# Optimization experiments

Hardware: AMD Instinct MI355X
Metric: run time of the kernel (lower is better)

The kernel has to match this reference:

```python
import jax, jax.numpy as jnp
import numpy as np

B, J, D = 512, 22, 3
HIDDEN = 512
OUT = J * D          # 66, flattened frame size
NCLS = 12
LENGTH = 64


def setup_inputs() -> dict:
    key = jax.random.key(0)
    ks = jax.random.split(key, 12)
    s = 0.05
    return {
        "inputs": jax.random.normal(ks[0], (B, J, D), dtype=jnp.float32),
        "labels": jax.random.randint(ks[1], (B,), 0, NCLS),
        "length": LENGTH,
        # LSTMCell params (torch layout: W_ih [4H, in], W_hh [4H, H], gate order i,f,g,o)
        "W_ih": jax.random.normal(ks[2], (4 * HIDDEN, OUT + NCLS), dtype=jnp.float32) * s,
        "W_hh": jax.random.normal(ks[3], (4 * HIDDEN, HIDDEN), dtype=jnp.float32) * s,
        "b_ih": jax.random.normal(ks[4], (4 * HIDDEN,), dtype=jnp.float32) * s,
        "b_hh": jax.random.normal(ks[5], (4 * HIDDEN,), dtype=jnp.float32) * s,
        # fc: hidden -> output
        "W_fc": jax.random.normal(ks[6], (OUT, HIDDEN), dtype=jnp.float32) * s,
        "b_fc": jax.random.normal(ks[7], (OUT,), dtype=jnp.float32) * s,
        # fc_inh / fc_inc: output -> hidden (initial state projections)
        "W_inh": jax.random.normal(ks[8], (HIDDEN, OUT), dtype=jnp.float32) * s,
        "b_inh": jax.random.normal(ks[9], (HIDDEN,), dtype=jnp.float32) * s,
        "W_inc": jax.random.normal(ks[10], (HIDDEN, OUT), dtype=jnp.float32) * s,
        "b_inc": jax.random.normal(ks[11], (HIDDEN,), dtype=jnp.float32) * s,
    }


def reference(inputs, labels, length, W_ih, W_hh, b_ih, b_hh, W_fc, b_fc,
              W_inh, b_inh, W_inc, b_inc):
    b, j, d = inputs.shape
    enc = jax.nn.one_hot(labels, NCLS, dtype=inputs.dtype)      # [B, NCLS]
    frame0 = inputs.reshape(b, j * d)                            # [B, OUT]
    h0 = frame0 @ W_inh.T + b_inh                                # [B, H]
    c0 = frame0 @ W_inc.T + b_inc                                # [B, H]
    frame = jnp.concatenate([frame0, enc], axis=-1)              # [B, OUT+NCLS]

    def step(carry, _):
        h, c, fr = carry
        gates = fr @ W_ih.T + b_ih + h @ W_hh.T + b_hh           # [B, 4H]
        i, f, g, o = jnp.split(gates, 4, axis=-1)                # torch gate order
        c_new = jax.nn.sigmoid(f) * c + jax.nn.sigmoid(i) * jnp.tanh(g)
        h_new = jax.nn.sigmoid(o) * jnp.tanh(c_new)
        out = h_new @ W_fc.T + b_fc                              # [B, OUT]
        fr_new = jnp.concatenate([out, enc], axis=-1)
        return (h_new, c_new, fr_new), out

    _, outs = jax.lax.scan(step, (h0, c0, frame), None, length=length)  # [L, B, OUT]
    return jnp.transpose(outs, (1, 0, 2)).reshape(b, length, j, d)
```

## Files before the change

### kernel.cpp

```cpp
#include <hip/hip_runtime.h>

#define OUTD 66
#define INW  78
#define FH   2048
#define LEN  64

typedef short bf16x8 __attribute__((ext_vector_type(8)));
typedef float f32x4  __attribute__((ext_vector_type(4)));
typedef unsigned int u32x4 __attribute__((ext_vector_type(4)));

__device__ __forceinline__ float bf2f(unsigned short u) {
  union { unsigned int i; float f; } v; v.i = ((unsigned int)u) << 16; return v.f;
}
__device__ __forceinline__ unsigned short f2bf(float f) {
  union { float f; unsigned int i; } v; v.f = f;
  unsigned int u = v.i;
  return (unsigned short)((u + 0x7fffu + ((u >> 16) & 1u)) >> 16);
}
__device__ __forceinline__ float sigm(float x) { return 1.f / (1.f + __expf(-x)); }
__device__ __forceinline__ float tanh_f(float x) { return 2.f / (1.f + __expf(-2.f * x)) - 1.f; }

__global__ __launch_bounds__(256) void k_initA(
    const float* __restrict__ W_hh, const float* __restrict__ W_ih,
    const float* __restrict__ W_fc, const float* __restrict__ b_ih,
    const float* __restrict__ b_hh, const float* __restrict__ b_fc,
    const float* __restrict__ inp, const float* __restrict__ W_inh,
    const float* __restrict__ b_inh, const float* __restrict__ W_inc,
    const float* __restrict__ b_inc,
    unsigned short* __restrict__ Weff, float* __restrict__ bias_eff,
    unsigned short* __restrict__ hbuf, float* __restrict__ c0,
    unsigned short* __restrict__ Wfc16, unsigned int* __restrict__ flags,
    unsigned int* __restrict__ flagsL)
{
  int tid = threadIdx.x, bid = blockIdx.x;
  if (bid < 256) {
    int nb = bid;
    int k = tid * 2;
    float acc[8][2];
    #pragma unroll
    for (int r = 0; r < 8; ++r) {
      int n = nb * 8 + r;
      acc[r][0] = W_hh[n * 512 + k];
      acc[r][1] = W_hh[n * 512 + k + 1];
    }
    for (int m = 0; m < OUTD; ++m) {
      float w0 = W_fc[m * 512 + k];
      float w1 = W_fc[m * 512 + k + 1];
      #pragma unroll
      for (int r = 0; r < 8; ++r) {
        float wih = W_ih[(nb * 8 + r) * INW + m];
        acc[r][0] += wih * w0;
        acc[r][1] += wih * w1;
      }
    }
    #pragma unroll
    for (int r = 0; r < 8; ++r) {
      int n = nb * 8 + r;
      unsigned int pack = (unsigned int)f2bf(acc[r][0]) | ((unsigned int)f2bf(acc[r][1]) << 16);
      *(unsigned int*)(Weff + n * 512 + k) = pack;
    }
    if (tid < 8) {
      int n = nb * 8 + tid;
      float a = b_ih[n] + b_hh[n];
      for (int m = 0; m < OUTD; ++m) a += b_fc[m] * W_ih[n * INW + m];
      bias_eff[n] = a;
    }
    if (nb == 0) {
      for (int i = tid; i < 512 * 16; i += 256) flags[i] = 0;
      for (int i = tid; i < 256 * 16; i += 256) flagsL[i] = 0;
    }
  } else {
    int nb = bid - 256;
    for (int r = 0; r < 2; ++r) {
      int b = nb * 2 + r;
      for (int half = 0; half < 2; ++half) {
        int c = tid + half * 256;
        float ha = b_inh[c], ca = b_inc[c];
        for (int m = 0; m < OUTD; ++m) {
          float f = inp[b * OUTD + m];
          ha += f * W_inh[c * OUTD + m];
          ca += f * W_inc[c * OUTD + m];
        }
        hbuf[((b >> 6) * 32 + (c >> 4)) * 1024 + (b & 63) * 16 + (c & 15)] = f2bf(ha);
        c0[b * 512 + c] = ca;
      }
    }
    if (nb == 0) {
      for (int i = tid; i < OUTD * 512; i += 256) Wfc16[i] = f2bf(W_fc[i]);
    }
  }
}

__global__ __launch_bounds__(128) void k_init2a(
    const float* __restrict__ inp, const unsigned short* __restrict__ hbuf,
    const float* __restrict__ W_fc, const float* __restrict__ b_fc,
    float* __restrict__ d0)
{
  int b = blockIdx.x, m = threadIdx.x;
  if (m >= OUTD) return;
  const unsigned short* hb = hbuf + (b >> 6) * 32768 + (b & 63) * 16;
  const float* wrow = W_fc + m * 512;
  float acc = 0.f;
  for (int k = 0; k < 512; ++k)
    acc += bf2f(hb[(k >> 4) * 1024 + (k & 15)]) * wrow[k];
  d0[b * OUTD + m] = inp[b * OUTD + m] - (acc + b_fc[m]);
}

__global__ __launch_bounds__(256) void k_init2b(
    const float* __restrict__ d0, const float* __restrict__ W_ih,
    float* __restrict__ corr0)
{
  __shared__ float ds[4][OUTD];
  int tid = threadIdx.x, b0 = blockIdx.x * 4;
  for (int i = tid; i < 4 * OUTD; i += 256) ds[i / OUTD][i % OUTD] = d0[b0 * OUTD + i];
  __syncthreads();
  for (int n = tid; n < FH; n += 256) {
    float a0 = 0, a1 = 0, a2 = 0, a3 = 0;
    const float* wr = W_ih + n * INW;
    for (int m = 0; m < OUTD; ++m) {
      float w = wr[m];
      a0 += ds[0][m] * w; a1 += ds[1][m] * w; a2 += ds[2][m] * w; a3 += ds[3][m] * w;
    }
    corr0[(b0 + 0) * FH + n] = a0;
    corr0[(b0 + 1) * FH + n] = a1;
    corr0[(b0 + 2) * FH + n] = a2;
    corr0[(b0 + 3) * FH + n] = a3;
  }
}

__global__ __launch_bounds__(256, 1) void k_main(
    const unsigned short* __restrict__ Weff, const float* __restrict__ bias_eff,
    unsigned short* __restrict__ hbuf, const float* __restrict__ c0,
    const float* __restrict__ corr0, const float* __restrict__ W_ih,
    const int* __restrict__ labels, const unsigned short* __restrict__ Wfc16,
    const float* __restrict__ b_fc, float* __restrict__ out,
    unsigned int* __restrict__ flags, unsigned int* __restrict__ flagsL)
{
  __shared__ __align__(16) unsigned short h_lds[64 * 512];

  int tid = threadIdx.x, bid = blockIdx.x;
  int w = tid >> 6, lane = tid & 63;
  int lc = lane & 15, kg = lane >> 4;
  unsigned int* xmap = flags + 4096;
  unsigned int* decp = flags + 4088;

  unsigned int xcd;
  asm volatile("s_getreg_b32 %0, hwreg(HW_REG_XCC_ID)" : "=s"(xcd));
  if (tid == 0)
    __hip_atomic_store(&xmap[bid * 16], xcd + 1u, __ATOMIC_RELAXED, __HIP_MEMORY_SCOPE_AGENT);

  if (bid == 0 && w == 0) {
    int okA = 1, okB = 1;
    #pragma unroll
    for (int i = 0; i < 4; ++i) {
      int b = lane + i * 64;
      unsigned int v, ra, rb;
      const unsigned int* xp = &xmap[b * 16];
      for (;;) { v = __hip_atomic_load(xp, __ATOMIC_RELAXED, __HIP_MEMORY_SCOPE_AGENT);
                 if (v) break; __builtin_amdgcn_s_sleep(1); }
      const unsigned int* pa = &xmap[(b & 7) * 16];
      for (;;) { ra = __hip_atomic_load(pa, __ATOMIC_RELAXED, __HIP_MEMORY_SCOPE_AGENT);
                 if (ra) break; __builtin_amdgcn_s_sleep(1); }
      const unsigned int* pb = &xmap[((b >> 5) << 5) * 16];
      for (;;) { rb = __hip_atomic_load(pb, __ATOMIC_RELAXED, __HIP_MEMORY_SCOPE_AGENT);
                 if (rb) break; __builtin_amdgcn_s_sleep(1); }
      okA &= (v == ra); okB &= (v == rb);
    }
    okA = __all(okA); okB = __all(okB);
    if (lane == 0) {
      unsigned int d = okA ? 1u : (okB ? 2u : 3u);
      __hip_atomic_store(decp, d, __ATOMIC_RELAXED, __HIP_MEMORY_SCOPE_AGENT);
    }
  }
  if (tid == 0) {
    unsigned int dd;
    for (;;) { dd = __hip_atomic_load(decp, __ATOMIC_RELAXED, __HIP_MEMORY_SCOPE_AGENT);
               if (dd) break; __builtin_amdgcn_s_sleep(1); }
    h_lds[0] = (unsigned short)dd;
  }
  __syncthreads();
  unsigned int dmode = h_lds[0];
  __syncthreads();

  int fast, mt, jt;
  if (dmode == 1u)      { fast = 1; mt = bid & 7;  jt = bid >> 3; }
  else if (dmode == 2u) { fast = 1; mt = bid >> 5; jt = bid & 31; }
  else                  { fast = 0; mt = bid & 7;  jt = bid >> 3; }

  int row0 = mt * 64, j0 = jt * 16;
  int hx0 = (w >> 1) * 8;
  int xloc = lc & 7;
  int G = lc >> 3;
  int hcol = j0 + hx0 + xloc;
  int rw0 = (w & 1) * 32;

  int sA = xloc;
  int tA16 = ((kg ^ sA) & 3) << 4;
  int ue64 = ((sA >> 2) & 1) << 6;
  int PA0 = (rw0 + lc) * 1024 + tA16 + ue64;
  int PA1 = PA0 + 16 * 1024;
  int PF  = (w * 16 + lc) * 1024 + tA16 + ue64;

  bf16x8 Bfrag[16][2];
  #pragma unroll
  for (int cg = 0; cg < 2; ++cg) {
    int n = (cg * 2 + G) * 512 + hcol;
    const unsigned short* p = Weff + n * 512 + kg * 8;
    #pragma unroll
    for (int i = 0; i < 16; ++i) Bfrag[i][cg] = *(const bf16x8*)(p + i * 32);
  }

  bf16x8 Wf[16];
  float fcb = 0.f;
  {
    int n = j0 + lc;
    if (jt < 5 && n < OUTD) {
      const unsigned short* p = Wfc16 + n * 512 + kg * 8;
      #pragma unroll
      for (int i = 0; i < 16; ++i) Wf[i] = *(const bf16x8*)(p + i * 32);
      fcb = b_fc[n];
    } else {
      bf16x8 z8 = {0, 0, 0, 0, 0, 0, 0, 0};
      #pragma unroll
      for (int i = 0; i < 16; ++i) Wf[i] = z8;
    }
  }

  int qsel = G * 2;
  float lt[4][4], creg[4];
  #pragma unroll
  for (int idx = 0; idx < 4; ++idx) {
    int rloc = rw0 + (idx >> 1) * 16 + kg * 4 + qsel + (idx & 1);
    int grow = row0 + rloc;
    int lab = labels[grow];
    #pragma unroll
    for (int gt = 0; gt < 4; ++gt) {
      int n = gt * 512 + hcol;
      lt[gt][idx] = bias_eff[n] + W_ih[n * INW + OUTD + lab];
    }
    creg[idx] = c0[grow * 512 + hcol];
  }

  const f32x4 z = {0.f, 0.f, 0.f, 0.f};
  unsigned int* myflag  = &flags[(mt * 32 + jt) * 16];
  unsigned int* myflagL = &flagsL[(mt * 32 + jt) * 16];
  int useL = 1;

  {
    const unsigned short* hsrc = hbuf + mt * 32768;
    #pragma unroll
    for (int i = 0; i < 16; ++i) {
      int n = tid + i * 256;
      int c = n >> 7, q = n & 127;
      int r = q >> 1, u = q & 1, g = c * 2 + u;
      *(u32x4*)(h_lds + r * 512 + ((g ^ (r & 7)) << 3)) =
          *(const u32x4*)(hsrc + n * 8);
    }
  }
  __syncthreads();

  for (int s = 0; s < LEN; ++s) {
    f32x4 acc00 = z, acc01 = z, acc10 = z, acc11 = z;
    #pragma unroll
    for (int i = 0; i < 16; ++i) {
      bf16x8 a0 = *(const bf16x8*)((const char*)h_lds + (PA0 ^ (i << 6)));
      bf16x8 a1 = *(const bf16x8*)((const char*)h_lds + (PA1 ^ (i << 6)));
      acc00 = __builtin_amdgcn_mfma_f32_16x16x32_bf16(a0, Bfrag[i][0], acc00, 0, 0, 0);
      acc10 = __builtin_amdgcn_mfma_f32_16x16x32_bf16(a1, Bfrag[i][0], acc10, 0, 0, 0);
      acc01 = __builtin_amdgcn_mfma_f32_16x16x32_bf16(a0, Bfrag[i][1], acc01, 0, 0, 0);
      acc11 = __builtin_amdgcn_mfma_f32_16x16x32_bf16(a1, Bfrag[i][1], acc11, 0, 0, 0);
    }

    f32x4 sh00, sh01, sh10, sh11;
    #pragma unroll
    for (int j = 0; j < 4; ++j) {
      sh00[j] = __shfl_xor(acc00[j], 8);
      sh01[j] = __shfl_xor(acc01[j], 8);
      sh10[j] = __shfl_xor(acc10[j], 8);
      sh11[j] = __shfl_xor(acc11[j], 8);
    }

    unsigned short hval[4];
    #pragma unroll
    for (int idx = 0; idx < 4; ++idx) {
      int jj = idx & 1, hh = idx >> 1;
      int qo = qsel + jj;
      float xi, xf, xg, xo;
      if (hh == 0) {
        xi = (G ? sh00[qo] : acc00[qo]);
        xf = (G ? acc00[qo] : sh00[qo]);
        xg = (G ? sh01[qo] : acc01[qo]);
        xo = (G ? acc01[qo] : sh01[qo]);
      } else {
        xi = (G ? sh10[qo] : acc10[qo]);
        xf = (G ? acc10[qo] : sh10[qo]);
        xg = (G ? sh11[qo] : acc11[qo]);
        xo = (G ? acc11[qo] : sh11[qo]);
      }
      xi += lt[0][idx]; xf += lt[1][idx]; xg += lt[2][idx]; xo += lt[3][idx];
      if (s == 0) {
        int rloc = rw0 + hh * 16 + kg * 4 + qo;
        const float* cr = corr0 + (long)(row0 + rloc) * FH + hcol;
        xi += cr[0]; xf += cr[512]; xg += cr[1024]; xo += cr[1536];
      }
      float cn = sigm(xf) * creg[idx] + sigm(xi) * tanh_f(xg);
      creg[idx] = cn;
      hval[idx] = f2bf(sigm(xo) * tanh_f(cn));
    }

    {
      unsigned int* hdst32 = (unsigned int*)(hbuf + ((s + 1) & 1) * 262144);
      int base32 = (mt * 32 + jt) * 512;
      int ceL = (hx0 >> 1) + (xloc >> 1);
      int odd = xloc & 1;
      unsigned int pk[2]; int ro[2]; int np = 0;
      #pragma unroll
      for (int idx = 0; idx < 4; ++idx) {
        unsigned int mine = hval[idx];
        unsigned int part = (unsigned int)__shfl_xor((int)mine, 1);
        unsigned int p = odd ? (part | (mine << 16)) : (mine | (part << 16));
        if ((idx >> 1) == odd) {
          int rloc = rw0 + (idx >> 1) * 16 + kg * 4 + qsel + (idx & 1);
          pk[np] = p; ro[np] = base32 + rloc * 8 + ceL; ++np;
        }
      }
      if (fast) {
        hdst32[ro[0]] = pk[0];
        hdst32[ro[1]] = pk[1];
      } else {
        __hip_atomic_store(&hdst32[ro[0]], pk[0], __ATOMIC_RELAXED, __HIP_MEMORY_SCOPE_AGENT);
        __hip_atomic_store(&hdst32[ro[1]], pk[1], __ATOMIC_RELAXED, __HIP_MEMORY_SCOPE_AGENT);
      }
    }

    __builtin_amdgcn_s_waitcnt(0);
    __syncthreads();
    if (tid == 0) {
      if (fast)
        *(volatile unsigned int*)myflagL = (unsigned int)(s + 1);
      __hip_atomic_store(myflag, (unsigned int)(s + 1),
                         __ATOMIC_RELAXED, __HIP_MEMORY_SCOPE_AGENT);
    }

    f32x4 fa = z;
    int dofc = (jt < 5) & (s >= 1);
    if (dofc) {
      #pragma unroll
      for (int i = 0; i < 16; ++i) {
        bf16x8 a = *(const bf16x8*)((const char*)h_lds + (PF ^ (i << 6)));
        fa = __builtin_amdgcn_mfma_f32_16x16x32_bf16(a, Wf[i], fa, 0, 0, 0);
      }
    }
    __syncthreads();

    {
      int gS = jt * 2 + (w >> 1);
      #pragma unroll
      for (int idx = 0; idx < 4; ++idx) {
        int rloc = rw0 + (idx >> 1) * 16 + kg * 4 + qsel + (idx & 1);
        h_lds[rloc * 512 + ((gS ^ (rloc & 7)) << 3) + xloc] = hval[idx];
      }
    }

    if (s < LEN - 1 || jt < 5) {
      const unsigned short* hbC = hbuf + ((s + 1) & 1) * 262144 + mt * 32768;
      int pidx = (mt * 32 + w * 8 + (lane & 7)) * 16;
      volatile const unsigned int* fL = flagsL + pidx;
      const unsigned int* fA = flags + pidx;
      unsigned int done = (w == (jt >> 3)) ? (1u << (jt & 7)) : 0u;
      int spins = 0;
      while (done != 0xffu) {
        unsigned int fv;
        int loc = fast & useL;
        if (loc) {
          asm volatile("buffer_inv\n\ts_waitcnt vmcnt(0)" ::: "memory");
          fv = *fL;
          if (++spins > 2048) useL = 0;
        } else {
          fv = __hip_atomic_load(fA, __ATOMIC_RELAXED, __HIP_MEMORY_SCOPE_AGENT);
        }
        unsigned int todo =
            ((unsigned int)__ballot((int)(fv >= (unsigned int)(s + 1))) & 0xffu) & ~done;
        if (!todo) { if (!loc) __builtin_amdgcn_s_sleep(1); continue; }
        if (!loc) __builtin_amdgcn_fence(__ATOMIC_ACQUIRE, "agent");

        u32x4 ta[8], tb[8];
        #pragma unroll
        for (int i = 0; i < 8; ++i) {
          if ((todo >> i) & 1u) {
            const unsigned short* cp = hbC + (w * 8 + i) * 1024 + lane * 8;
            ta[i] = *(const u32x4*)cp;
            tb[i] = *(const u32x4*)(cp + 512);
          }
        }
        int r0_ = lane >> 1, u = lane & 1, r1_ = 32 + r0_;
        #pragma unroll
        for (int i = 0; i < 8; ++i) {
          if ((todo >> i) & 1u) {
            int c2 = (w * 8 + i) * 2 + u;
            *(u32x4*)(h_lds + r0_ * 512 + ((c2 ^ (r0_ & 7)) << 3)) = ta[i];
            *(u32x4*)(h_lds + r1_ * 512 + ((c2 ^ (r1_ & 7)) << 3)) = tb[i];
          }
        }
        done |= todo;
      }
    }

    if (dofc) {
      int c = j0 + lc;
      if (c < OUTD) {
        #pragma unroll
        for (int q = 0; q < 4; ++q) {
          int b = row0 + w * 16 + kg * 4 + q;
          out[((long)b * 64 + (s - 1)) * OUTD + c] = fa[q] + fcb;
        }
      }
    }
    __syncthreads();
  }

  if (jt < 5) {
    f32x4 fa = z;
    #pragma unroll
    for (int i = 0; i < 16; ++i) {
      bf16x8 a = *(const bf16x8*)((const char*)h_lds + (PF ^ (i << 6)));
      fa = __builtin_amdgcn_mfma_f32_16x16x32_bf16(a, Wf[i], fa, 0, 0, 0);
    }
    int c = j0 + lc;
    if (c < OUTD) {
      #pragma unroll
      for (int q = 0; q < 4; ++q) {
        int b = row0 + w * 16 + kg * 4 + q;
        out[((long)b * 64 + 63) * OUTD + c] = fa[q] + fcb;
      }
    }
  }
}

extern "C" void kernel_launch(void* const* d_in, const int* in_sizes, int n_in,
                              void* d_out, int out_size, void* d_ws, size_t ws_size,
                              hipStream_t stream) {
  (void)in_sizes; (void)n_in; (void)out_size; (void)ws_size;
  const float* inp   = (const float*)d_in[0];
  const int*   labels= (const int*)d_in[1];
  const float* W_ih  = (const float*)d_in[3];
  const float* W_hh  = (const float*)d_in[4];
  const float* b_ih  = (const float*)d_in[5];
  const float* b_hh  = (const float*)d_in[6];
  const float* W_fc  = (const float*)d_in[7];
  const float* b_fc  = (const float*)d_in[8];
  const float* W_inh = (const float*)d_in[9];
  const float* b_inh = (const float*)d_in[10];
  const float* W_inc = (const float*)d_in[11];
  const float* b_inc = (const float*)d_in[12];

  char* ws = (char*)d_ws;
  unsigned short* Weff = (unsigned short*)(ws + 0);
  float* bias_eff      = (float*)(ws + 2097152);
  unsigned short* hbuf = (unsigned short*)(ws + 2105344);
  float* c0            = (float*)(ws + 3153920);
  float* corr0         = (float*)(ws + 4202496);
  float* d0            = (float*)(ws + 8396800);
  unsigned int* flags  = (unsigned int*)(ws + 8531968);
  unsigned short* Wfc16= (unsigned short*)(ws + 8564736);
  unsigned int* flagsL = (unsigned int*)(ws + 8632320);

  k_initA<<<512, 256, 0, stream>>>(W_hh, W_ih, W_fc, b_ih, b_hh, b_fc,
                                   inp, W_inh, b_inh, W_inc, b_inc,
                                   Weff, bias_eff, hbuf, c0, Wfc16, flags, flagsL);
  k_init2a<<<512, 128, 0, stream>>>(inp, hbuf, W_fc, b_fc, d0);
  k_init2b<<<128, 256, 0, stream>>>(d0, W_ih, corr0);

  k_main<<<256, 256, 0, stream>>>(Weff, bias_eff, hbuf, c0, corr0, W_ih, labels,
                                  Wfc16, b_fc, (float*)d_out, flags, flagsL);
}
```

Baseline: 457.6 us.

## Replace per-block local flags with atomic-OR bitmask per step for peer readiness

Producers now signal readiness by atomically OR-ing their bit into a per-(group, step) mask word instead of writing a per-block flag. Consumers poll one mask word with a single lane's returning atomic instead of a 64-lane ballot over eight flags. The fallback to agent-scope flags now triggers after fewer spins, and the poll loop always sleeps between empty polls. The LDS writeback of the block's own h values is also packed into 32-bit stores. The change trades eight flag loads per poll for one atomic round trip, which adds atomic traffic on the shared mask words.

```diff
diff --git a/kernel.cpp b/kernel.cpp
--- a/kernel.cpp
+++ b/kernel.cpp
@@ -19,6 +19,16 @@
 }
 __device__ __forceinline__ float sigm(float x) { return 1.f / (1.f + __expf(-x)); }
 __device__ __forceinline__ float tanh_f(float x) { return 2.f / (1.f + __expf(-2.f * x)) - 1.f; }
+
+__device__ __forceinline__ unsigned int atom_or_ret(unsigned int* p, unsigned int d) {
+  unsigned int r;
+  asm volatile("global_atomic_or %0, %1, %2, off sc0\n\ts_waitcnt vmcnt(0)"
+               : "=&v"(r) : "v"(p), "v"(d) : "memory");
+  return r;
+}
+__device__ __forceinline__ void atom_or(unsigned int* p, unsigned int d) {
+  asm volatile("global_atomic_or %0, %1, off" :: "v"(p), "v"(d) : "memory");
+}
 
 __global__ __launch_bounds__(256) void k_initA(
     const float* __restrict__ W_hh, const float* __restrict__ W_ih,
@@ -143,6 +153,7 @@
   int lc = lane & 15, kg = lane >> 4;
   unsigned int* xmap = flags + 4096;
   unsigned int* decp = flags + 4088;
+  unsigned int* maskW = flagsL;
 
   unsigned int xcd;
   asm volatile("s_getreg_b32 %0, hwreg(HW_REG_XCC_ID)" : "=s"(xcd));
@@ -242,9 +253,7 @@
   }
 
   const f32x4 z = {0.f, 0.f, 0.f, 0.f};
-  unsigned int* myflag  = &flags[(mt * 32 + jt) * 16];
-  unsigned int* myflagL = &flagsL[(mt * 32 + jt) * 16];
-  int useL = 1;
+  unsigned int* myflag = &flags[(mt * 32 + jt) * 16];
 
   {
     const unsigned short* hsrc = hbuf + mt * 32768;
@@ -308,12 +317,13 @@
       hval[idx] = f2bf(sigm(xo) * tanh_f(cn));
     }
 
+    unsigned int pkS[2]; int rlS[2];
     {
       unsigned int* hdst32 = (unsigned int*)(hbuf + ((s + 1) & 1) * 262144);
       int base32 = (mt * 32 + jt) * 512;
       int ceL = (hx0 >> 1) + (xloc >> 1);
       int odd = xloc & 1;
-      unsigned int pk[2]; int ro[2]; int np = 0;
+      int np = 0;
       #pragma unroll
       for (int idx = 0; idx < 4; ++idx) {
         unsigned int mine = hval[idx];
@@ -321,15 +331,17 @@
         unsigned int p = odd ? (part | (mine << 16)) : (mine | (part << 16));
         if ((idx >> 1) == odd) {
           int rloc = rw0 + (idx >> 1) * 16 + kg * 4 + qsel + (idx & 1);
-          pk[np] = p; ro[np] = base32 + rloc * 8 + ceL; ++np;
+          pkS[np] = p; rlS[np] = rloc; ++np;
         }
       }
       if (fast) {
-        hdst32[ro[0]] = pk[0];
-        hdst32[ro[1]] = pk[1];
+        hdst32[base32 + rlS[0] * 8 + ceL] = pkS[0];
+        hdst32[base32 + rlS[1] * 8 + ceL] = pkS[1];
       } else {
-        __hip_atomic_store(&hdst32[ro[0]], pk[0], __ATOMIC_RELAXED, __HIP_MEMORY_SCOPE_AGENT);
-        __hip_atomic_store(&hdst32[ro[1]], pk[1], __ATOMIC_RELAXED, __HIP_MEMORY_SCOPE_AGENT);
+        __hip_atomic_store(&hdst32[base32 + rlS[0] * 8 + ceL], pkS[0],
+                           __ATOMIC_RELAXED, __HIP_MEMORY_SCOPE_AGENT);
+        __hip_atomic_store(&hdst32[base32 + rlS[1] * 8 + ceL], pkS[1],
+                           __ATOMIC_RELAXED, __HIP_MEMORY_SCOPE_AGENT);
       }
     }
 
@@ -337,7 +349,7 @@
     __syncthreads();
     if (tid == 0) {
       if (fast)
-        *(volatile unsigned int*)myflagL = (unsigned int)(s + 1);
+        atom_or(&maskW[(mt * 4 + (jt >> 3)) * 64 + s], 1u << (jt & 7));
       __hip_atomic_store(myflag, (unsigned int)(s + 1),
                          __ATOMIC_RELAXED, __HIP_MEMORY_SCOPE_AGENT);
     }
@@ -355,34 +367,39 @@
 
     {
       int gS = jt * 2 + (w >> 1);
-      #pragma unroll
-      for (int idx = 0; idx < 4; ++idx) {
-        int rloc = rw0 + (idx >> 1) * 16 + kg * 4 + qsel + (idx & 1);
-        h_lds[rloc * 512 + ((gS ^ (rloc & 7)) << 3) + xloc] = hval[idx];
+      unsigned int* l32 = (unsigned int*)h_lds;
+      #pragma unroll
+      for (int t = 0; t < 2; ++t) {
+        int rl = rlS[t];
+        l32[rl * 256 + ((gS ^ (rl & 7)) << 2) + (xloc >> 1)] = pkS[t];
       }
     }
 
     if (s < LEN - 1 || jt < 5) {
       const unsigned short* hbC = hbuf + ((s + 1) & 1) * 262144 + mt * 32768;
-      int pidx = (mt * 32 + w * 8 + (lane & 7)) * 16;
-      volatile const unsigned int* fL = flagsL + pidx;
-      const unsigned int* fA = flags + pidx;
-      unsigned int done = (w == (jt >> 3)) ? (1u << (jt & 7)) : 0u;
+      unsigned int mydone = (w == (jt >> 3)) ? (1u << (jt & 7)) : 0u;
+      const unsigned int* fA = flags + (mt * 32 + w * 8 + (lane & 7)) * 16;
+      unsigned int* mg = &maskW[(mt * 4 + w) * 64 + s];
+      int agentMode = !fast;
       int spins = 0;
-      while (done != 0xffu) {
-        unsigned int fv;
-        int loc = fast & useL;
-        if (loc) {
+      while (mydone != 0xffu) {
+        unsigned int avail;
+        if (!agentMode) {
+          unsigned int v = 0;
+          if (lane == 0) v = atom_or_ret(mg, 0u);
+          avail = (unsigned int)__shfl((int)v, 0);
+          if (++spins > 1024) agentMode = 1;
+        } else {
+          unsigned int fv = __hip_atomic_load(fA, __ATOMIC_RELAXED, __HIP_MEMORY_SCOPE_AGENT);
+          avail = (unsigned int)__ballot((int)(fv >= (unsigned int)(s + 1))) & 0xffu;
+        }
+        unsigned int todo = avail & ~mydone;
+        if (!todo) { __builtin_amdgcn_s_sleep(1); continue; }
+
+        if (agentMode)
+          __builtin_amdgcn_fence(__ATOMIC_ACQUIRE, "agent");
+        else
           asm volatile("buffer_inv\n\ts_waitcnt vmcnt(0)" ::: "memory");
-          fv = *fL;
-          if (++spins > 2048) useL = 0;
-        } else {
-          fv = __hip_atomic_load(fA, __ATOMIC_RELAXED, __HIP_MEMORY_SCOPE_AGENT);
-        }
-        unsigned int todo =
-            ((unsigned int)__ballot((int)(fv >= (unsigned int)(s + 1))) & 0xffu) & ~done;
-        if (!todo) { if (!loc) __builtin_amdgcn_s_sleep(1); continue; }
-        if (!loc) __builtin_amdgcn_fence(__ATOMIC_ACQUIRE, "agent");
 
         u32x4 ta[8], tb[8];
         #pragma unroll
@@ -402,7 +419,7 @@
             *(u32x4*)(h_lds + r1_ * 512 + ((c2 ^ (r1_ & 7)) << 3)) = tb[i];
           }
         }
-        done |= todo;
+        mydone |= todo;
       }
     }
 
```

After: 450.8 us. About the same (-1.5%).

## Replace per-block flag polling with atomic counter barrier per row group

Applied to the files above, without the earlier changes.

Instead of every wave polling 8 peer flags and copying h tiles incrementally as each peer finishes, each block atomically increments a per-step counter and the last arriver publishes a group-done flag. One wave spins on that single flag, then all waves bulk-load the full h slice from global memory into LDS. This cuts polling traffic and removes the per-wave ballot loop, and it also drops the block's own local LDS write of h. The cost is losing the overlap of early-finisher copies and adding an atomic round trip on the critical path. The local-h write removal depends on the global buffer holding the block's own output.

```diff
diff --git a/kernel.cpp b/kernel.cpp
--- a/kernel.cpp
+++ b/kernel.cpp
@@ -19,6 +19,13 @@
 }
 __device__ __forceinline__ float sigm(float x) { return 1.f / (1.f + __expf(-x)); }
 __device__ __forceinline__ float tanh_f(float x) { return 2.f / (1.f + __expf(-2.f * x)) - 1.f; }
+
+__device__ __forceinline__ unsigned int atom_add_ret(unsigned int* p, unsigned int d) {
+  unsigned int r;
+  asm volatile("global_atomic_add %0, %1, %2, off sc0\n\ts_waitcnt vmcnt(0)"
+               : "=&v"(r) : "v"(p), "v"(d) : "memory");
+  return r;
+}
 
 __global__ __launch_bounds__(256) void k_initA(
     const float* __restrict__ W_hh, const float* __restrict__ W_ih,
@@ -242,9 +249,8 @@
   }
 
   const f32x4 z = {0.f, 0.f, 0.f, 0.f};
-  unsigned int* myflag  = &flags[(mt * 32 + jt) * 16];
-  unsigned int* myflagL = &flagsL[(mt * 32 + jt) * 16];
-  int useL = 1;
+  unsigned int* myflag = &flags[(mt * 32 + jt) * 16];
+  int agentMode = !fast;
 
   {
     const unsigned short* hsrc = hbuf + mt * 32768;
@@ -335,78 +341,28 @@
 
     __builtin_amdgcn_s_waitcnt(0);
     __syncthreads();
-    if (tid == 0) {
-      if (fast)
-        *(volatile unsigned int*)myflagL = (unsigned int)(s + 1);
+    if (tid == 128) {
+      if (fast) {
+        unsigned int* cntp = &flagsL[mt * 64 + ((s + 1) & 3)];
+        unsigned int old = atom_add_ret(cntp, 1u);
+        if (old == 31u) {
+          *(volatile unsigned int*)&flagsL[mt * 64 + 32 + ((s + 1) & 3)] =
+              (unsigned int)(s + 1);
+          *(volatile unsigned int*)&flagsL[mt * 64 + ((s + 3) & 3)] = 0u;
+        }
+      }
       __hip_atomic_store(myflag, (unsigned int)(s + 1),
                          __ATOMIC_RELAXED, __HIP_MEMORY_SCOPE_AGENT);
     }
 
-    f32x4 fa = z;
     int dofc = (jt < 5) & (s >= 1);
     if (dofc) {
+      f32x4 fa = z;
       #pragma unroll
       for (int i = 0; i < 16; ++i) {
         bf16x8 a = *(const bf16x8*)((const char*)h_lds + (PF ^ (i << 6)));
         fa = __builtin_amdgcn_mfma_f32_16x16x32_bf16(a, Wf[i], fa, 0, 0, 0);
       }
-    }
-    __syncthreads();
-
-    {
-      int gS = jt * 2 + (w >> 1);
-      #pragma unroll
-      for (int idx = 0; idx < 4; ++idx) {
-        int rloc = rw0 + (idx >> 1) * 16 + kg * 4 + qsel + (idx & 1);
-        h_lds[rloc * 512 + ((gS ^ (rloc & 7)) << 3) + xloc] = hval[idx];
-      }
-    }
-
-    if (s < LEN - 1 || jt < 5) {
-      const unsigned short* hbC = hbuf + ((s + 1) & 1) * 262144 + mt * 32768;
-      int pidx = (mt * 32 + w * 8 + (lane & 7)) * 16;
-      volatile const unsigned int* fL = flagsL + pidx;
-      const unsigned int* fA = flags + pidx;
-      unsigned int done = (w == (jt >> 3)) ? (1u << (jt & 7)) : 0u;
-      int spins = 0;
-      while (done != 0xffu) {
-        unsigned int fv;
-        int loc = fast & useL;
-        if (loc) {
-          asm volatile("buffer_inv\n\ts_waitcnt vmcnt(0)" ::: "memory");
-          fv = *fL;
-          if (++spins > 2048) useL = 0;
-        } else {
-          fv = __hip_atomic_load(fA, __ATOMIC_RELAXED, __HIP_MEMORY_SCOPE_AGENT);
-        }
-        unsigned int todo =
-            ((unsigned int)__ballot((int)(fv >= (unsigned int)(s + 1))) & 0xffu) & ~done;
-        if (!todo) { if (!loc) __builtin_amdgcn_s_sleep(1); continue; }
-        if (!loc) __builtin_amdgcn_fence(__ATOMIC_ACQUIRE, "agent");
-
-        u32x4 ta[8], tb[8];
-        #pragma unroll
-        for (int i = 0; i < 8; ++i) {
-          if ((todo >> i) & 1u) {
-            const unsigned short* cp = hbC + (w * 8 + i) * 1024 + lane * 8;
-            ta[i] = *(const u32x4*)cp;
-            tb[i] = *(const u32x4*)(cp + 512);
-          }
-        }
-        int r0_ = lane >> 1, u = lane & 1, r1_ = 32 + r0_;
-        #pragma unroll
-        for (int i = 0; i < 8; ++i) {
-          if ((todo >> i) & 1u) {
-            int c2 = (w * 8 + i) * 2 + u;
-            *(u32x4*)(h_lds + r0_ * 512 + ((c2 ^ (r0_ & 7)) << 3)) = ta[i];
-            *(u32x4*)(h_lds + r1_ * 512 + ((c2 ^ (r1_ & 7)) << 3)) = tb[i];
-          }
-        }
-        done |= todo;
-      }
-    }
-
-    if (dofc) {
       int c = j0 + lc;
       if (c < OUTD) {
         #pragma unroll
@@ -414,6 +370,53 @@
           int b = row0 + w * 16 + kg * 4 + q;
           out[((long)b * 64 + (s - 1)) * OUTD + c] = fa[q] + fcb;
         }
+      }
+    }
+
+    int needE = (s < LEN - 1 || jt < 5);
+    if (w == 3 && needE) {
+      if (!agentMode) {
+        volatile const unsigned int* gop =
+            (volatile const unsigned int*)&flagsL[mt * 64 + 32 + ((s + 1) & 3)];
+        int spins = 0;
+        for (;;) {
+          asm volatile("buffer_inv\n\ts_waitcnt vmcnt(0)" ::: "memory");
+          if (*gop == (unsigned int)(s + 1)) break;
+          if (++spins > 1024) { agentMode = 1; break; }
+          __builtin_amdgcn_s_sleep(1);
+        }
+      }
+      if (agentMode) {
+        const unsigned int* fA = flags + (mt * 32 + (lane & 31)) * 16;
+        for (;;) {
+          unsigned int fv = __hip_atomic_load(fA, __ATOMIC_RELAXED, __HIP_MEMORY_SCOPE_AGENT);
+          if (__all((int)(fv >= (unsigned int)(s + 1)))) break;
+          __builtin_amdgcn_s_sleep(1);
+        }
+      }
+    }
+    __syncthreads();
+
+    if (needE) {
+      if (fast) {
+        asm volatile("buffer_inv\n\ts_waitcnt vmcnt(0)" ::: "memory");
+      } else {
+        __builtin_amdgcn_fence(__ATOMIC_ACQUIRE, "agent");
+      }
+      const unsigned short* hbC = hbuf + ((s + 1) & 1) * 262144 + mt * 32768;
+      u32x4 ta[8], tb[8];
+      #pragma unroll
+      for (int i = 0; i < 8; ++i) {
+        const unsigned short* cp = hbC + (w * 8 + i) * 1024 + lane * 8;
+        ta[i] = *(const u32x4*)cp;
+        tb[i] = *(const u32x4*)(cp + 512);
+      }
+      int r0_ = lane >> 1, u = lane & 1, r1_ = 32 + r0_;
+      #pragma unroll
+      for (int i = 0; i < 8; ++i) {
+        int c2 = (w * 8 + i) * 2 + u;
+        *(u32x4*)(h_lds + r0_ * 512 + ((c2 ^ (r0_ & 7)) << 3)) = ta[i];
+        *(u32x4*)(h_lds + r1_ * 512 + ((c2 ^ (r1_ & 7)) << 3)) = tb[i];
       }
     }
     __syncthreads();
```

New measurement: 464.0 us. About the same (+1.4%).
